# Optimization experiments

Hardware: AMD Instinct MI355X
Metric: run time of the kernel (lower is better)

The kernel has to match this reference:

```python
import jax, jax.numpy as jnp
import numpy as np

DIM = 384
HEADS = 8
RATES = (0.5, 0.75)  # sparse_rates
EPS = 1e-12  # torch F.normalize default eps


def _dwconv3x3(x, w):
    # depthwise 3x3, padding=1; w: [3*dim, 1, 3, 3]
    return jax.lax.conv_general_dilated(
        x, w, window_strides=(1, 1), padding=((1, 1), (1, 1)),
        feature_group_count=w.shape[0],
        dimension_numbers=('NCHW', 'OIHW', 'NCHW'))


def setup_inputs() -> dict:
    key = jax.random.key(0)
    ks = jax.random.split(key, 5)
    dim = DIM
    x = jax.random.normal(ks[0], (4, dim, 128, 128), jnp.float32)
    qkv_w = jax.random.normal(ks[1], (3 * dim, dim), jnp.float32) * 0.05   # 1x1 conv
    dw_w = jax.random.normal(ks[2], (3 * dim, 1, 3, 3), jnp.float32) * 0.1  # depthwise 3x3
    proj_w = jax.random.normal(ks[3], (dim, dim), jnp.float32) * 0.05       # 1x1 conv
    temperature = jnp.ones((HEADS, 1, 1), jnp.float32)
    attns = jnp.full((len(RATES),), 0.2, jnp.float32)
    return {"x": x, "qkv_w": qkv_w, "dw_w": dw_w, "proj_w": proj_w,
            "temperature": temperature, "attns": attns}


def reference(x, qkv_w, dw_w, proj_w, temperature, attns) -> jnp.ndarray:
    b, c, h, w = x.shape
    qkv = jnp.einsum('bchw,oc->bohw', x, qkv_w)  # 1x1 conv, no bias
    qkv = _dwconv3x3(qkv, dw_w)
    q, k, v = jnp.split(qkv, 3, axis=1)

    def heads(t):  # b (head c) h w -> b head c (h w)
        return t.reshape(b, HEADS, c // HEADS, h * w)

    q, k, v = heads(q), heads(k), heads(v)
    q = q / jnp.maximum(jnp.linalg.norm(q, axis=-1, keepdims=True), EPS)
    k = k / jnp.maximum(jnp.linalg.norm(k, axis=-1, keepdims=True), EPS)
    C = q.shape[2]
    attn = jnp.einsum('bhcn,bhdn->bhcd', q, k) * temperature  # [b, head, C, C]

    out = jnp.zeros_like(v)  # [b, head, C, HW]
    for i, rate in enumerate(RATES):
        kk = int(C * rate)
        _, idx = jax.lax.top_k(attn, kk)                      # [b, head, C, kk]
        mask = jax.nn.one_hot(idx, C, dtype=attn.dtype).sum(-2) > 0  # scatter 1s
        attn = jnp.where(mask, attn, -jnp.inf)
        attn = jax.nn.softmax(attn, axis=-1)  # NOTE: original reuses softmaxed attn next iter
        out = out + jnp.einsum('bhcd,bhdn->bhcn', attn, v) * attns[i]

    out = out.reshape(b, c, h, w)  # b head c (hw) -> b (head c) h w
    return jnp.einsum('bchw,oc->bohw', out, proj_w)
```

## Files before the change

kernel.cpp:

```cpp
#include <hip/hip_runtime.h>
#include <math.h>

#define HW     16384
#define WIDTH  128
#define CDIM   384
#define QKVC   1152
#define HEADS  8
#define CH     48
#define NSPLIT 32
#define GK     384

typedef unsigned short u16;
typedef short bf16x8 __attribute__((ext_vector_type(8)));
typedef float f32x4 __attribute__((ext_vector_type(4)));

__device__ __forceinline__ void split2(float x, u16& h, u16& l) {
    union { float f; unsigned u; } a, b, c;
    a.f = x;
    unsigned hu = (a.u + 0x7fffu + ((a.u >> 16) & 1u)) & 0xffff0000u;
    b.u = hu;
    h = (u16)(hu >> 16);
    c.f = x - b.f;
    l = (u16)((c.u + 0x7fffu + ((c.u >> 16) & 1u)) >> 16);
}

__device__ __forceinline__ void gload16(const void* g, void* l) {
    __builtin_amdgcn_global_load_lds((const __attribute__((address_space(1))) unsigned int*)g,
                                     (__attribute__((address_space(3))) unsigned int*)l, 16, 0, 0);
}

__global__ __launch_bounds__(512)
void mfma_gemm(const u16* __restrict__ Ah, const u16* __restrict__ Al,
               const u16* __restrict__ Bh, const u16* __restrict__ Bl,
               float* __restrict__ C, int nmb,
               long abs_, long bbs, long cbs)
{
    extern __shared__ char smem[];
    const int tot = gridDim.x * gridDim.y;
    const int per = tot >> 3;
    const int fl  = blockIdx.x + gridDim.x * blockIdx.y;
    const int f2  = (fl & 7) * per + (fl >> 3);
    const int nblk = f2 / nmb, mblk = f2 % nmb;
    const int b = blockIdx.z;
    Ah += (long)b * abs_; Al += (long)b * abs_;
    Bh += (long)b * bbs;  Bl += (long)b * bbs;
    C  += (long)b * cbs;
    const int m0 = mblk * 128, n0 = nblk * 256;

    const int tid  = threadIdx.x;
    const int wave = tid >> 6, lane = tid & 63;
    const int lr = lane & 15, lg = lane >> 4;
    const int wm = wave >> 2, wn = wave & 3;
    const int wb = wave * 1024;

    const int sr  = tid >> 2;
    const int kxs = (tid & 3) ^ ((sr >> 1) & 3);

    f32x4 acc[4][4];
#pragma unroll
    for (int i = 0; i < 4; ++i)
#pragma unroll
        for (int j = 0; j < 4; ++j) acc[i][j] = (f32x4){0.f, 0.f, 0.f, 0.f};

#define STAGE(bufsel, kt) do {                                                     \
        char* LL = smem + (bufsel) * 49152;                                        \
        const long ko = (long)(kt) * 32 + kxs * 8;                                 \
        gload16(Ah + (long)(m0 + sr) * GK + ko,        LL + wb);                   \
        gload16(Al + (long)(m0 + sr) * GK + ko,        LL + 8192  + wb);           \
        gload16(Bh + (long)(n0 + sr) * GK + ko,        LL + 16384 + wb);           \
        gload16(Bh + (long)(n0 + 128 + sr) * GK + ko,  LL + 24576 + wb);           \
        gload16(Bl + (long)(n0 + sr) * GK + ko,        LL + 32768 + wb);           \
        gload16(Bl + (long)(n0 + 128 + sr) * GK + ko,  LL + 40960 + wb);           \
    } while (0)

    STAGE(0, 0);
    STAGE(1, 1);
    int cur = 0;
    for (int kt = 0; kt < 12; ++kt) {
        if (kt < 11) asm volatile("s_waitcnt vmcnt(6)" ::: "memory");
        else         asm volatile("s_waitcnt vmcnt(0)" ::: "memory");
        __builtin_amdgcn_s_barrier();

        const char* L = smem + cur * 49152;
        bf16x8 af[4][2], bf[4][2];
#pragma unroll
        for (int mi = 0; mi < 4; ++mi) {
            int r = wm * 64 + mi * 16 + lr;
            int off = r * 64 + (((lg ^ (r >> 1)) & 3) << 4);
            af[mi][0] = *(const bf16x8*)(L + off);
            af[mi][1] = *(const bf16x8*)(L + 8192 + off);
        }
#pragma unroll
        for (int ni = 0; ni < 4; ++ni) {
            int r = wn * 64 + ni * 16 + lr;
            int off = r * 64 + (((lg ^ (r >> 1)) & 3) << 4);
            bf[ni][0] = *(const bf16x8*)(L + 16384 + off);
            bf[ni][1] = *(const bf16x8*)(L + 32768 + off);
        }
        asm volatile("s_waitcnt lgkmcnt(0)" ::: "memory");
        __builtin_amdgcn_sched_barrier(0);
        __builtin_amdgcn_s_barrier();
        if (kt < 10) STAGE(cur, kt + 2);

        __builtin_amdgcn_s_setprio(1);
#pragma unroll
        for (int mi = 0; mi < 4; ++mi)
#pragma unroll
            for (int ni = 0; ni < 4; ++ni) {
                acc[mi][ni] = __builtin_amdgcn_mfma_f32_16x16x32_bf16(af[mi][0], bf[ni][0], acc[mi][ni], 0, 0, 0);
                acc[mi][ni] = __builtin_amdgcn_mfma_f32_16x16x32_bf16(af[mi][0], bf[ni][1], acc[mi][ni], 0, 0, 0);
                acc[mi][ni] = __builtin_amdgcn_mfma_f32_16x16x32_bf16(af[mi][1], bf[ni][0], acc[mi][ni], 0, 0, 0);
            }
        __builtin_amdgcn_s_setprio(0);
        cur ^= 1;
    }
#undef STAGE

#pragma unroll
    for (int mi = 0; mi < 4; ++mi)
#pragma unroll
        for (int ni = 0; ni < 4; ++ni) {
            int row = m0 + wm * 64 + mi * 16 + lg * 4;
            int col = n0 + wn * 64 + ni * 16 + lr;
            float* cp = C + (long)row * HW + col;
            cp[0]          = acc[mi][ni][0];
            cp[(long)HW]   = acc[mi][ni][1];
            cp[2L * HW]    = acc[mi][ni][2];
            cp[3L * HW]    = acc[mi][ni][3];
        }
}

__global__ __launch_bounds__(256)
void convT_kernel(const float* __restrict__ in, u16* __restrict__ oh, u16* __restrict__ ol,
                  long ibs, long obs)
{
    const int b = blockIdx.z;
    in += (long)b * ibs; oh += (long)b * obs; ol += (long)b * obs;
    __shared__ float t[32][33];
    const int p0 = blockIdx.x * 32, c0 = blockIdx.y * 32;
    const int ty = threadIdx.x >> 5, tx = threadIdx.x & 31;
#pragma unroll
    for (int it = 0; it < 4; ++it) {
        int c = ty + it * 8;
        t[c][tx] = in[(long)(c0 + c) * HW + p0 + tx];
    }
    __syncthreads();
    const int cp = threadIdx.x & 15;
    const int py = threadIdx.x >> 4;
#pragma unroll
    for (int half = 0; half < 2; ++half) {
        int p = py + half * 16;
        u16 h0, l0, h1, l1;
        split2(t[2 * cp][p], h0, l0);
        split2(t[2 * cp + 1][p], h1, l1);
        long o = (long)(p0 + p) * CDIM + c0 + 2 * cp;
        *(ushort2*)&oh[o] = (ushort2){h0, h1};
        *(ushort2*)&ol[o] = (ushort2){l0, l1};
    }
}

__global__ __launch_bounds__(256)
void convA_kernel(const float* __restrict__ in, u16* __restrict__ oh, u16* __restrict__ ol, int n)
{
    int i = blockIdx.x * 256 + threadIdx.x;
    if (i < n) split2(in[i], oh[i], ol[i]);
}

__global__ __launch_bounds__(256)
void dwconv_kernel(const float* __restrict__ in, const float* __restrict__ w,
                   float* __restrict__ out)
{
    const long base = (long)blockIdx.y * QKVC * HW;
    const int idx = blockIdx.x * 256 + threadIdx.x;
    const int ch = idx >> 11;
    const int wi = idx & 2047;
    const int y = wi >> 4, x0 = (wi & 15) * 8;
    const float* wp = w + ch * 9;
    const float* ip = in + base + (long)ch * HW;
    float o[8] = {0.f, 0.f, 0.f, 0.f, 0.f, 0.f, 0.f, 0.f};
#pragma unroll
    for (int dy = -1; dy <= 1; ++dy) {
        int yy = y + dy;
        if ((unsigned)yy >= 128u) continue;
        const float* rp = ip + yy * WIDTH + x0;
        float4 a  = *(const float4*)rp;
        float4 bq = *(const float4*)(rp + 4);
        float v[10] = { (x0 > 0) ? rp[-1] : 0.f,
                        a.x, a.y, a.z, a.w, bq.x, bq.y, bq.z, bq.w,
                        (x0 < 120) ? rp[8] : 0.f };
        float w0 = wp[(dy + 1) * 3], w1 = wp[(dy + 1) * 3 + 1], w2 = wp[(dy + 1) * 3 + 2];
#pragma unroll
        for (int j = 0; j < 8; ++j)
            o[j] = fmaf(w0, v[j], fmaf(w1, v[j + 1], fmaf(w2, v[j + 2], o[j])));
    }
    float* op = out + base + (long)ch * HW + y * WIDTH + x0;
    *(float4*)op       = (float4){o[0], o[1], o[2], o[3]};
    *(float4*)(op + 4) = (float4){o[4], o[5], o[6], o[7]};
}

__global__ __launch_bounds__(256)
void attn_partial_kernel(const float* __restrict__ dw, float* __restrict__ part,
                         float* __restrict__ part2, long ps, long p2s)
{
    const int split = blockIdx.x, h = blockIdx.y, b = blockIdx.z;
    const int n0 = split * (HW / NSPLIT);
    const float* qbase = dw + ((long)b * QKVC + h * CH) * HW;
    const float* kbase = dw + ((long)b * QKVC + CDIM + h * CH) * HW;
    __shared__ float qs[64][CH];
    __shared__ float ks[64][CH];
    const int tid = threadIdx.x;
    const int tr = tid >> 4, tc = tid & 15;
    const int c0 = tr * 3, d0 = tc * 3;
    float acc[3][3] = {{0.f}};
    float qss[3] = {0.f, 0.f, 0.f}, kss[3] = {0.f, 0.f, 0.f};
    const int cA = tid >> 4;
    const int nq = (tid & 15) * 4;
    for (int ns = 0; ns < HW / NSPLIT; ns += 64) {
        __syncthreads();
#pragma unroll
        for (int t = 0; t < 3; ++t) {
            int c = cA + t * 16;
            float4 qv = *(const float4*)(qbase + (long)c * HW + n0 + ns + nq);
            float4 kv = *(const float4*)(kbase + (long)c * HW + n0 + ns + nq);
            qs[nq + 0][c] = qv.x; qs[nq + 1][c] = qv.y;
            qs[nq + 2][c] = qv.z; qs[nq + 3][c] = qv.w;
            ks[nq + 0][c] = kv.x; ks[nq + 1][c] = kv.y;
            ks[nq + 2][c] = kv.z; ks[nq + 3][c] = kv.w;
            qss[t] += qv.x * qv.x + qv.y * qv.y + qv.z * qv.z + qv.w * qv.w;
            kss[t] += kv.x * kv.x + kv.y * kv.y + kv.z * kv.z + kv.w * kv.w;
        }
        __syncthreads();
#pragma unroll 8
        for (int n = 0; n < 64; ++n) {
            float q0 = qs[n][c0], q1 = qs[n][c0 + 1], q2 = qs[n][c0 + 2];
            float k0 = ks[n][d0], k1 = ks[n][d0 + 1], k2 = ks[n][d0 + 2];
            acc[0][0] = fmaf(q0, k0, acc[0][0]); acc[0][1] = fmaf(q0, k1, acc[0][1]); acc[0][2] = fmaf(q0, k2, acc[0][2]);
            acc[1][0] = fmaf(q1, k0, acc[1][0]); acc[1][1] = fmaf(q1, k1, acc[1][1]); acc[1][2] = fmaf(q1, k2, acc[1][2]);
            acc[2][0] = fmaf(q2, k0, acc[2][0]); acc[2][1] = fmaf(q2, k1, acc[2][1]); acc[2][2] = fmaf(q2, k2, acc[2][2]);
        }
    }
#pragma unroll
    for (int m = 1; m < 16; m <<= 1) {
#pragma unroll
        for (int t = 0; t < 3; ++t) {
            qss[t] += __shfl_xor(qss[t], m);
            kss[t] += __shfl_xor(kss[t], m);
        }
    }
    if ((tid & 15) == 0) {
        float* p2 = part2 + (long)b * p2s + ((long)h * NSPLIT + split) * 96;
#pragma unroll
        for (int t = 0; t < 3; ++t) {
            p2[cA + t * 16]      = qss[t];
            p2[48 + cA + t * 16] = kss[t];
        }
    }
    float* po = part + (long)b * ps + ((long)h * NSPLIT + split) * (CH * CH);
#pragma unroll
    for (int i = 0; i < 3; ++i)
#pragma unroll
        for (int j = 0; j < 3; ++j)
            po[(c0 + i) * CH + d0 + j] = acc[i][j];
}

__global__ __launch_bounds__(256)
void attn_reduce_kernel(const float* __restrict__ part, const float* __restrict__ part2,
                        const float* __restrict__ temp, float* __restrict__ attn,
                        long ps, long p2s, long as_)
{
    const int seg = blockIdx.x, h = blockIdx.y, b = blockIdx.z;
    const float* pp = part + (long)b * ps + (long)h * NSPLIT * (CH * CH);
    const float* p2 = part2 + (long)b * p2s + (long)h * NSPLIT * 96;
    __shared__ float sinv[96];
    if (threadIdx.x < 96) {
        float s = 0.f;
        for (int sp = 0; sp < NSPLIT; ++sp) s += p2[sp * 96 + threadIdx.x];
        sinv[threadIdx.x] = 1.f / fmaxf(sqrtf(s), 1e-12f);
    }
    __syncthreads();
    const float t = temp[h];
    const int idx = seg * 256 + threadIdx.x;
    const int c = idx / CH, d = idx % CH;
    float s = 0.f;
    for (int sp = 0; sp < NSPLIT; ++sp) s += pp[sp * (CH * CH) + idx];
    attn[(long)b * as_ + (long)h * (CH * CH) + idx] = s * sinv[c] * sinv[48 + d] * t;
}

__global__ __launch_bounds__(256)
void maskw_kernel(const float* __restrict__ attn, const float* __restrict__ attns,
                  float* __restrict__ W, long as_, long ws_)
{
    const int h = blockIdx.y, b = blockIdx.z;
    const int wave = threadIdx.x >> 6, lane = threadIdx.x & 63;
    const int r = blockIdx.x * 4 + wave;
    const float* ap = attn + (long)b * as_ + (long)h * (CH * CH) + (long)r * CH;
    float a = (lane < CH) ? ap[lane] : -3.4e38f;

    int rank = 0;
#pragma unroll
    for (int j = 0; j < CH; ++j) {
        float aj = __shfl(a, j);
        rank += (aj > a) || (aj == a && j < lane);
    }
    const bool keep = (lane < CH) && (rank < 24);
    float m = keep ? a : -3.4e38f;
#pragma unroll
    for (int o = 32; o > 0; o >>= 1) m = fmaxf(m, __shfl_xor(m, o));
    float e = keep ? expf(a - m) : 0.f;
    float s = e;
#pragma unroll
    for (int o = 32; o > 0; o >>= 1) s += __shfl_xor(s, o);
    const float A1 = e / s;

    int rank2 = 0;
#pragma unroll
    for (int j = 0; j < CH; ++j) {
        float aj = __shfl(A1, j);
        rank2 += (aj > A1) || (aj == A1 && j < lane);
    }
    const bool keep2 = (lane < CH) && (rank2 < 36);
    float m2 = keep2 ? A1 : -3.4e38f;
#pragma unroll
    for (int o = 32; o > 0; o >>= 1) m2 = fmaxf(m2, __shfl_xor(m2, o));
    float e2 = keep2 ? expf(A1 - m2) : 0.f;
    float s2 = e2;
#pragma unroll
    for (int o = 32; o > 0; o >>= 1) s2 += __shfl_xor(s2, o);

    if (lane < CH)
        W[(long)b * ws_ + (long)h * (CH * CH) + (long)r * CH + lane] =
            attns[0] * A1 + attns[1] * (e2 / s2);
}

__global__ __launch_bounds__(256)
void mbuild_kernel(const float* __restrict__ P, const float* __restrict__ W,
                   u16* __restrict__ Mh, u16* __restrict__ Ml, long ws_, long ms)
{
    const int b = blockIdx.y;
    const int idx = blockIdx.x * 256 + threadIdx.x;
    const int o = idx / CDIM, col = idx % CDIM;
    const int h = col / CH, d = col % CH;
    const float* wp = W + (long)b * ws_ + (long)h * (CH * CH) + d;
    const float* pp = P + (long)o * CDIM + h * CH;
    float s = 0.f;
#pragma unroll
    for (int c = 0; c < CH; ++c) s = fmaf(pp[c], wp[c * CH], s);
    u16 hh, ll;
    split2(s, hh, ll);
    Mh[(long)b * ms + idx] = hh;
    Ml[(long)b * ms + idx] = ll;
}

extern "C" void kernel_launch(void* const* d_in, const int* in_sizes, int n_in,
                              void* d_out, int out_size, void* d_ws, size_t ws_size,
                              hipStream_t stream)
{
    const float* x      = (const float*)d_in[0];
    const float* qkv_w  = (const float*)d_in[1];
    const float* dw_w   = (const float*)d_in[2];
    const float* proj_w = (const float*)d_in[3];
    const float* temp   = (const float*)d_in[4];
    const float* attns  = (const float*)d_in[5];
    float* out = (float*)d_out;

    const size_t perbB = (size_t)QKVC * HW * 4;
    auto need = [&](int nb) -> size_t {
        return (size_t)nb * 2 * perbB + 4u * QKVC * CDIM + 4096;
    };
    int NB = 4;
    while (NB > 1 && need(NB) > ws_size) NB >>= 1;

    const long fstride = (long)(perbB / 4);
    const long ustride = (long)(perbB / 2);

    const size_t PART_B  = 27u << 20;
    const size_t PART2_B = (29u << 20) + (512u << 10);
    const size_t ATT_B   = 30u << 20;
    const size_t WM_B    = 31u << 20;
    const size_t MH_B    = 32u << 20;
    const size_t ML_B    = 33u << 20;

    char* buf1 = (char*)d_ws;
    char* buf2 = buf1 + (size_t)NB * perbB;
    u16* Ah = (u16*)(buf2 + (size_t)NB * perbB);
    u16* Al = Ah + (size_t)QKVC * CDIM;

    convA_kernel<<<dim3((QKVC * CDIM + 255) / 256), 256, 0, stream>>>(qkv_w, Ah, Al, QKVC * CDIM);

    for (int b0 = 0; b0 < 4; b0 += NB) {
        const int nb = NB;
        float* pre = (float*)buf1;
        float* dwb = (float*)buf2;
        u16* xt_h = (u16*)buf2;                u16* xt_l = xt_h + (size_t)HW * CDIM;
        u16* vt_h = (u16*)buf1;                u16* vt_l = vt_h + (size_t)HW * CDIM;
        float* part  = (float*)(buf1 + PART_B);
        float* part2 = (float*)(buf1 + PART2_B);
        float* attn  = (float*)(buf1 + ATT_B);
        float* Wm    = (float*)(buf1 + WM_B);
        u16* Mh = (u16*)(buf1 + MH_B);
        u16* Ml = (u16*)(buf1 + ML_B);

        convT_kernel<<<dim3(HW / 32, CDIM / 32, nb), 256, 0, stream>>>(
            x + (size_t)b0 * CDIM * HW, xt_h, xt_l, (long)CDIM * HW, ustride);
        mfma_gemm<<<dim3(HW / 256, QKVC / 128, nb), 512, 98304, stream>>>(
            Ah, Al, xt_h, xt_l, pre, QKVC / 128, 0L, ustride, fstride);
        dwconv_kernel<<<dim3(QKVC * HW / 8 / 256, nb), 256, 0, stream>>>(pre, dw_w, dwb);
        attn_partial_kernel<<<dim3(NSPLIT, HEADS, nb), 256, 0, stream>>>(dwb, part, part2,
                                                                         fstride, fstride);
        attn_reduce_kernel<<<dim3(9, HEADS, nb), 256, 0, stream>>>(part, part2, temp, attn,
                                                                   fstride, fstride, fstride);
        maskw_kernel<<<dim3(12, HEADS, nb), 256, 0, stream>>>(attn, attns, Wm, fstride, fstride);
        mbuild_kernel<<<dim3(CDIM * CDIM / 256, nb), 256, 0, stream>>>(proj_w, Wm, Mh, Ml,
                                                                       fstride, ustride);
        convT_kernel<<<dim3(HW / 32, CDIM / 32, nb), 256, 0, stream>>>(
            dwb + (size_t)2 * CDIM * HW, vt_h, vt_l, fstride, ustride);
        mfma_gemm<<<dim3(HW / 256, CDIM / 128, nb), 512, 98304, stream>>>(
            Mh, Ml, vt_h, vt_l, out + (size_t)b0 * CDIM * HW, CDIM / 128,
            ustride, ustride, (long)CDIM * HW);
    }
}
```

Baseline: 696.9 us.

## Fuse V depthwise conv with transpose/split and shrink GEMM tile to 128x128

Adds a kernel that computes the depthwise conv for the V channels and writes the transposed bf16 hi/lo split directly. This removes the fp32 V write plus the separate convT pass. The main dwconv now covers only the Q/K channels. Separately, the MFMA GEMM moves from 512-thread 128x256 tiles to 256-thread 128x128 tiles with 64KB of LDS, doubling the grid and possibly raising occupancy at the cost of more B-operand reloads. The fused kernel's 2-byte strided stores (384 threads per pixel row) may coalesce reasonably but issue 16 scalar stores per thread.

```diff
diff --git a/kernel.cpp b/kernel.cpp
--- a/kernel.cpp
+++ b/kernel.cpp
@@ -29,7 +29,7 @@
                                      (__attribute__((address_space(3))) unsigned int*)l, 16, 0, 0);
 }
 
-__global__ __launch_bounds__(512)
+__global__ __launch_bounds__(256)
 void mfma_gemm(const u16* __restrict__ Ah, const u16* __restrict__ Al,
                const u16* __restrict__ Bh, const u16* __restrict__ Bl,
                float* __restrict__ C, int nmb,
@@ -45,16 +45,16 @@
     Ah += (long)b * abs_; Al += (long)b * abs_;
     Bh += (long)b * bbs;  Bl += (long)b * bbs;
     C  += (long)b * cbs;
-    const int m0 = mblk * 128, n0 = nblk * 256;
+    const int m0 = mblk * 128, n0 = nblk * 128;
 
     const int tid  = threadIdx.x;
     const int wave = tid >> 6, lane = tid & 63;
     const int lr = lane & 15, lg = lane >> 4;
-    const int wm = wave >> 2, wn = wave & 3;
-    const int wb = wave * 1024;
-
-    const int sr  = tid >> 2;
-    const int kxs = (tid & 3) ^ ((sr >> 1) & 3);
+    const int wm = wave >> 1, wn = wave & 1;
+
+    const int srow = tid >> 2;
+    const int kc   = tid & 3;
+    const int sw   = kc ^ ((srow >> 1) & 3);
 
     f32x4 acc[4][4];
 #pragma unroll
@@ -62,26 +62,27 @@
 #pragma unroll
         for (int j = 0; j < 4; ++j) acc[i][j] = (f32x4){0.f, 0.f, 0.f, 0.f};
 
-#define STAGE(bufsel, kt) do {                                                     \
-        char* LL = smem + (bufsel) * 49152;                                        \
-        const long ko = (long)(kt) * 32 + kxs * 8;                                 \
-        gload16(Ah + (long)(m0 + sr) * GK + ko,        LL + wb);                   \
-        gload16(Al + (long)(m0 + sr) * GK + ko,        LL + 8192  + wb);           \
-        gload16(Bh + (long)(n0 + sr) * GK + ko,        LL + 16384 + wb);           \
-        gload16(Bh + (long)(n0 + 128 + sr) * GK + ko,  LL + 24576 + wb);           \
-        gload16(Bl + (long)(n0 + sr) * GK + ko,        LL + 32768 + wb);           \
-        gload16(Bl + (long)(n0 + 128 + sr) * GK + ko,  LL + 40960 + wb);           \
+#define STAGE(bs, kt) do { char* LL = smem + (bs) * 32768;                          \
+        const long ko = (long)(kt) * 32 + sw * 8;                                   \
+        gload16(Ah + (long)(m0 + srow) * GK      + ko, LL + tid * 16);              \
+        gload16(Ah + (long)(m0 + 64 + srow) * GK + ko, LL + 4096  + tid * 16);      \
+        gload16(Al + (long)(m0 + srow) * GK      + ko, LL + 8192  + tid * 16);      \
+        gload16(Al + (long)(m0 + 64 + srow) * GK + ko, LL + 12288 + tid * 16);      \
+        gload16(Bh + (long)(n0 + srow) * GK      + ko, LL + 16384 + tid * 16);      \
+        gload16(Bh + (long)(n0 + 64 + srow) * GK + ko, LL + 20480 + tid * 16);      \
+        gload16(Bl + (long)(n0 + srow) * GK      + ko, LL + 24576 + tid * 16);      \
+        gload16(Bl + (long)(n0 + 64 + srow) * GK + ko, LL + 28672 + tid * 16);      \
     } while (0)
 
     STAGE(0, 0);
     STAGE(1, 1);
-    int cur = 0;
+#pragma unroll
     for (int kt = 0; kt < 12; ++kt) {
-        if (kt < 11) asm volatile("s_waitcnt vmcnt(6)" ::: "memory");
+        if (kt < 11) asm volatile("s_waitcnt vmcnt(8)" ::: "memory");
         else         asm volatile("s_waitcnt vmcnt(0)" ::: "memory");
         __builtin_amdgcn_s_barrier();
 
-        const char* L = smem + cur * 49152;
+        const char* L = smem + (kt & 1) * 32768;
         bf16x8 af[4][2], bf[4][2];
 #pragma unroll
         for (int mi = 0; mi < 4; ++mi) {
@@ -95,12 +96,12 @@
             int r = wn * 64 + ni * 16 + lr;
             int off = r * 64 + (((lg ^ (r >> 1)) & 3) << 4);
             bf[ni][0] = *(const bf16x8*)(L + 16384 + off);
-            bf[ni][1] = *(const bf16x8*)(L + 32768 + off);
+            bf[ni][1] = *(const bf16x8*)(L + 24576 + off);
         }
         asm volatile("s_waitcnt lgkmcnt(0)" ::: "memory");
         __builtin_amdgcn_sched_barrier(0);
         __builtin_amdgcn_s_barrier();
-        if (kt < 10) STAGE(cur, kt + 2);
+        if (kt + 2 < 12) STAGE(kt & 1, kt + 2);
 
         __builtin_amdgcn_s_setprio(1);
 #pragma unroll
@@ -112,7 +113,6 @@
                 acc[mi][ni] = __builtin_amdgcn_mfma_f32_16x16x32_bf16(af[mi][1], bf[ni][0], acc[mi][ni], 0, 0, 0);
             }
         __builtin_amdgcn_s_setprio(0);
-        cur ^= 1;
     }
 #undef STAGE
 
@@ -196,6 +196,43 @@
     float* op = out + base + (long)ch * HW + y * WIDTH + x0;
     *(float4*)op       = (float4){o[0], o[1], o[2], o[3]};
     *(float4*)(op + 4) = (float4){o[4], o[5], o[6], o[7]};
+}
+
+__global__ __launch_bounds__(384)
+void dwconv_vT_kernel(const float* __restrict__ in, const float* __restrict__ w,
+                      u16* __restrict__ oh, u16* __restrict__ ol, long ibs, long obs)
+{
+    const int b = blockIdx.y;
+    const int c = threadIdx.x;
+    const int p0 = blockIdx.x * 8;
+    const int y = p0 >> 7, x0 = p0 & 127;
+    const float* ip = in + (long)b * ibs + (long)(768 + c) * HW;
+    const float* wp = w + (768 + c) * 9;
+    float o[8] = {0.f, 0.f, 0.f, 0.f, 0.f, 0.f, 0.f, 0.f};
+#pragma unroll
+    for (int dy = -1; dy <= 1; ++dy) {
+        int yy = y + dy;
+        if ((unsigned)yy >= 128u) continue;
+        const float* rp = ip + yy * WIDTH + x0;
+        float4 a  = *(const float4*)rp;
+        float4 bq = *(const float4*)(rp + 4);
+        float v[10] = { (x0 > 0) ? rp[-1] : 0.f,
+                        a.x, a.y, a.z, a.w, bq.x, bq.y, bq.z, bq.w,
+                        (x0 < 120) ? rp[8] : 0.f };
+        float w0 = wp[(dy + 1) * 3], w1 = wp[(dy + 1) * 3 + 1], w2 = wp[(dy + 1) * 3 + 2];
+#pragma unroll
+        for (int j = 0; j < 8; ++j)
+            o[j] = fmaf(w0, v[j], fmaf(w1, v[j + 1], fmaf(w2, v[j + 2], o[j])));
+    }
+    u16* ph = oh + (long)b * obs + (long)p0 * CDIM + c;
+    u16* pl = ol + (long)b * obs + (long)p0 * CDIM + c;
+#pragma unroll
+    for (int j = 0; j < 8; ++j) {
+        u16 hh, ll;
+        split2(o[j], hh, ll);
+        ph[(long)j * CDIM] = hh;
+        pl[(long)j * CDIM] = ll;
+    }
 }
 
 __global__ __launch_bounds__(256)
@@ -392,7 +429,8 @@
         float* pre = (float*)buf1;
         float* dwb = (float*)buf2;
         u16* xt_h = (u16*)buf2;                u16* xt_l = xt_h + (size_t)HW * CDIM;
-        u16* vt_h = (u16*)buf1;                u16* vt_l = vt_h + (size_t)HW * CDIM;
+        u16* vt_h = (u16*)(dwb + (size_t)768 * HW);
+        u16* vt_l = vt_h + (size_t)CDIM * HW;
         float* part  = (float*)(buf1 + PART_B);
         float* part2 = (float*)(buf1 + PART2_B);
         float* attn  = (float*)(buf1 + ATT_B);
@@ -402,9 +440,11 @@
 
         convT_kernel<<<dim3(HW / 32, CDIM / 32, nb), 256, 0, stream>>>(
             x + (size_t)b0 * CDIM * HW, xt_h, xt_l, (long)CDIM * HW, ustride);
-        mfma_gemm<<<dim3(HW / 256, QKVC / 128, nb), 512, 98304, stream>>>(
+        mfma_gemm<<<dim3(HW / 128, QKVC / 128, nb), 256, 65536, stream>>>(
             Ah, Al, xt_h, xt_l, pre, QKVC / 128, 0L, ustride, fstride);
-        dwconv_kernel<<<dim3(QKVC * HW / 8 / 256, nb), 256, 0, stream>>>(pre, dw_w, dwb);
+        dwconv_kernel<<<dim3(768 * HW / 8 / 256, nb), 256, 0, stream>>>(pre, dw_w, dwb);
+        dwconv_vT_kernel<<<dim3(HW / 8, nb), 384, 0, stream>>>(pre, dw_w, vt_h, vt_l,
+                                                               fstride, ustride);
         attn_partial_kernel<<<dim3(NSPLIT, HEADS, nb), 256, 0, stream>>>(dwb, part, part2,
                                                                          fstride, fstride);
         attn_reduce_kernel<<<dim3(9, HEADS, nb), 256, 0, stream>>>(part, part2, temp, attn,
@@ -412,9 +452,7 @@
         maskw_kernel<<<dim3(12, HEADS, nb), 256, 0, stream>>>(attn, attns, Wm, fstride, fstride);
         mbuild_kernel<<<dim3(CDIM * CDIM / 256, nb), 256, 0, stream>>>(proj_w, Wm, Mh, Ml,
                                                                        fstride, ustride);
-        convT_kernel<<<dim3(HW / 32, CDIM / 32, nb), 256, 0, stream>>>(
-            dwb + (size_t)2 * CDIM * HW, vt_h, vt_l, fstride, ustride);
-        mfma_gemm<<<dim3(HW / 256, CDIM / 128, nb), 512, 98304, stream>>>(
+        mfma_gemm<<<dim3(HW / 128, CDIM / 128, nb), 256, 65536, stream>>>(
             Mh, Ml, vt_h, vt_l, out + (size_t)b0 * CDIM * HW, CDIM / 128,
             ustride, ustride, (long)CDIM * HW);
     }
```

Measured after the change: 772.7 us. 1.11x slower.
